# Optimization experiments

Measured on AMD Instinct MI355X. Metric: run time of the kernel, lower is better.

Reference implementation:

```python
import jax, jax.numpy as jnp
import numpy as np

B, T = 4, 8
H, W = 120, 160
NON_SEM = 4
CAT = 16
MAP_CH = NON_SEM + CAT          # 20 map channels
FEAT_CH = 2 * NON_SEM + CAT     # 24 feature channels
RES = 5.0                       # cm per map cell
GLOBAL_M, LOCAL_M = 960, 240    # map_size/resolution, and /downscale
M2 = LOCAL_M * LOCAL_M
HFOV = 79.0
CAM_H_CM = 88.0
VISION_CM = 100 * RES           # vision_range cells -> cm
AGENT_R2 = 2.0 ** 2
EXPLORE_R2 = 3.0 ** 2
FX = W / (2.0 * float(np.tan(np.deg2rad(HFOV) / 2.0)))
FY = FX
CX, CY = W / 2.0, H / 2.0

LOCAL_POSE0 = jnp.array([LOCAL_M * RES / 2, LOCAL_M * RES / 2, 0.0], jnp.float32)
GLOBAL_POSE0 = jnp.array([GLOBAL_M * RES / 2, GLOBAL_M * RES / 2, 0.0], jnp.float32)
OFF = (GLOBAL_M - LOCAL_M) // 2
BOUNDS0 = jnp.array([OFF, OFF + LOCAL_M, OFF, OFF + LOCAL_M], jnp.int32)
ORIGINS0 = jnp.array([OFF * RES, OFF * RES, 0.0], jnp.float32)


def _splat1(flat, w):  # scatter-add scalar weights into the flattened local grid
    return jnp.zeros((M2,), jnp.float32).at[flat].add(w)


def _splatC(flat, vals):  # vals [C, N] -> [C, M2]
    return jnp.zeros((vals.shape[0], M2), jnp.float32).at[:, flat].add(vals)


def _step(carry, xs):
    lmap, gmap, lpose, gpose, bounds, origins = carry
    obs, delta, cam_T, done, upd = xs
    doneb = done != 0
    # per-env reset on episode end (init_map_and_pose_for_env)
    lmap = jnp.where(doneb[:, None, None, None], 0.0, lmap)
    gmap = jnp.where(doneb[:, None, None, None], 0.0, gmap)
    lpose = jnp.where(doneb[:, None], LOCAL_POSE0, lpose)
    gpose = jnp.where(doneb[:, None], GLOBAL_POSE0, gpose)
    bounds = jnp.where(doneb[:, None], BOUNDS0, bounds)
    origins = jnp.where(doneb[:, None], ORIGINS0, origins)

    # dead-reckoning pose update (delta in agent frame)
    th = jnp.deg2rad(lpose[:, 2])
    dx = delta[:, 0] * jnp.cos(th) - delta[:, 1] * jnp.sin(th)
    dy = delta[:, 0] * jnp.sin(th) + delta[:, 1] * jnp.cos(th)
    lpose = lpose + jnp.stack([dx, dy, delta[:, 2]], -1)

    # depth -> camera-frame point cloud (cm)
    depth = obs[:, 3] * 400.0 + 50.0  # [B,H,W]
    sem = obs[:, NON_SEM:]            # [B,CAT,H,W]
    uu = (jnp.arange(W, dtype=jnp.float32) - CX)[None, None, :]
    vv = (CY - jnp.arange(H, dtype=jnp.float32))[None, :, None]
    pts = jnp.stack([uu * depth / FX, vv * depth / FY, depth, jnp.ones_like(depth)], -1)
    pts = jnp.einsum('bij,bhwj->bhwi', cam_T, pts)  # camera extrinsics
    x_f, y_l, z_u = pts[..., 2], -pts[..., 0], pts[..., 1] + CAM_H_CM

    # agent frame -> local map frame
    th2 = jnp.deg2rad(lpose[:, 2])[:, None, None]
    wx = lpose[:, 0][:, None, None] + x_f * jnp.cos(th2) - y_l * jnp.sin(th2)
    wy = lpose[:, 1][:, None, None] + x_f * jnp.sin(th2) + y_l * jnp.cos(th2)
    ix = jnp.floor(wx / RES).astype(jnp.int32)
    iy = jnp.floor(wy / RES).astype(jnp.int32)
    valid = (depth > 25.0) & (depth < VISION_CM) & (ix >= 0) & (ix < LOCAL_M) & (iy >= 0) & (iy < LOCAL_M)
    flat = (jnp.clip(iy, 0, LOCAL_M - 1) * LOCAL_M + jnp.clip(ix, 0, LOCAL_M - 1)).reshape(B, -1)
    vm = valid.reshape(B, -1).astype(jnp.float32)
    obst_w = vm * ((z_u > 25.0) & (z_u < 150.0)).reshape(B, -1).astype(jnp.float32)

    exp_grid = jax.vmap(_splat1)(flat, vm).reshape(B, LOCAL_M, LOCAL_M)
    obst_grid = jax.vmap(_splat1)(flat, obst_w).reshape(B, LOCAL_M, LOCAL_M)
    sem_grid = jax.vmap(_splatC)(flat, sem.reshape(B, CAT, -1) * vm[:, None, :]).reshape(B, CAT, LOCAL_M, LOCAL_M)

    # agent location / been-close disks
    g = jnp.arange(LOCAL_M, dtype=jnp.float32)
    dxg = g[None, None, :] - (lpose[:, 0] / RES)[:, None, None]
    dyg = g[None, :, None] - (lpose[:, 1] / RES)[:, None, None]
    d2 = dxg * dxg + dyg * dyg
    agent = (d2 <= AGENT_R2).astype(jnp.float32)
    close = (d2 <= EXPLORE_R2).astype(jnp.float32)

    lmap = jnp.concatenate([
        jnp.maximum(lmap[:, 0], jnp.clip(obst_grid, 0.0, 1.0))[:, None],
        jnp.maximum(lmap[:, 1], jnp.clip(exp_grid, 0.0, 1.0))[:, None],
        agent[:, None],
        jnp.maximum(lmap[:, 3], close)[:, None],
        jnp.maximum(lmap[:, NON_SEM:], jnp.clip(sem_grid, 0.0, 1.0)),
    ], axis=1)

    # fuse local window into global map for envs flagged for update
    y1, x1 = bounds[:, 0], bounds[:, 2]
    crop = jax.vmap(lambda gm, y, x: jax.lax.dynamic_slice(gm, (0, y, x), (MAP_CH, LOCAL_M, LOCAL_M)))(gmap, y1, x1)
    updb = (upd != 0)[:, None, None, None]
    fused = jnp.where(updb, jnp.maximum(crop, lmap), crop)
    gmap = jax.vmap(lambda gm, c, y, x: jax.lax.dynamic_update_slice(gm, c, (0, y, x)))(gmap, fused, y1, x1)
    gpose = jnp.where((upd != 0)[:, None], lpose + origins, gpose)

    feats = jnp.concatenate([lmap[:, :NON_SEM], fused[:, :NON_SEM], lmap[:, NON_SEM:]], axis=1)
    return (lmap, gmap, lpose, gpose, bounds, origins), (feats, lpose, gpose, bounds, origins)


def _forward(obs_seq, pose_delta, cam_poses, init_local_map, init_global_map,
             init_local_pose, init_global_pose, init_origins,
             done_flags, update_flags, init_bounds):
    xs = (obs_seq.swapaxes(0, 1), pose_delta.swapaxes(0, 1), cam_poses.swapaxes(0, 1),
          done_flags.swapaxes(0, 1), update_flags.swapaxes(0, 1))
    carry0 = (init_local_map, init_global_map, init_local_pose, init_global_pose, init_bounds, init_origins)
    carry, ys = jax.lax.scan(_step, carry0, xs)
    feats, lp, gp, bnds, orgs = ys
    return (feats.swapaxes(0, 1), carry[0], carry[1], lp.swapaxes(0, 1), gp.swapaxes(0, 1),
            bnds.swapaxes(0, 1), orgs.swapaxes(0, 1))


def setup_inputs() -> dict:
    key = jax.random.key(0)
    ks = jax.random.split(key, 5)
    obs_seq = jax.random.uniform(ks[0], (B, T, MAP_CH, H, W), jnp.float32)
    pose_delta = jax.random.normal(ks[1], (B, T, 3), jnp.float32) * jnp.array([10.0, 2.0, 5.0], jnp.float32)
    cam_poses = jnp.eye(4, dtype=jnp.float32)[None, None] + 0.02 * jax.random.normal(ks[2], (B, T, 4, 4), jnp.float32)
    done_flags = jax.random.randint(ks[3], (B, T), 0, 2, jnp.int32)
    update_flags = jax.random.randint(ks[4], (B, T), 0, 2, jnp.int32)
    return {
        'obs_seq': obs_seq,
        'pose_delta': pose_delta,
        'done_flags': done_flags,
        'update_flags': update_flags,
        'cam_poses': cam_poses,
        'init_local_map': jnp.zeros((B, MAP_CH, LOCAL_M, LOCAL_M), jnp.float32),
        'init_global_map': jnp.zeros((B, MAP_CH, GLOBAL_M, GLOBAL_M), jnp.float32),
        'init_local_pose': jnp.tile(LOCAL_POSE0[None], (B, 1)),
        'init_global_pose': jnp.tile(GLOBAL_POSE0[None], (B, 1)),
        'init_bounds': jnp.tile(BOUNDS0[None], (B, 1)),
        'init_origins': jnp.tile(ORIGINS0[None], (B, 1)),
    }


def reference(obs_seq, pose_delta, done_flags, update_flags, cam_poses,
              init_local_map, init_global_map, init_local_pose, init_global_pose,
              init_bounds, init_origins):
    return _forward(obs_seq, pose_delta, cam_poses, init_local_map, init_global_map,
                    init_local_pose, init_global_pose, init_origins,
                    done_flags, update_flags, init_bounds)
```

## Files before the change

kernel.cpp:

```cpp
#include <hip/hip_runtime.h>
#include <math.h>

#define Bn 4
#define Tn 8
#define Hn 120
#define Wn 160
#define HWn (Hn * Wn)
#define NON_SEMn 4
#define CATn 16
#define MAP_CHn 20
#define FEAT_CHn 24
#define LOCAL_Mn 240
#define GLOBAL_Mn 960
#define M2n (LOCAL_Mn * LOCAL_Mn)
#define TBMn (Tn * Bn * M2n)
#define Pn (Tn * Bn * HWn)
#define NBLK_SCAN 1800

#define DEG2RADf ((float)0.017453292519943295)

#define OUT_FEATS 0
#define OUT_LMAP  44236800
#define OUT_GMAP  48844800
#define OUT_LP    122572800
#define OUT_GP    122572896
#define OUT_BNDS  122572992
#define OUT_ORGS  122573120

#define WS_LPOSE  0
#define WS_ANYD   96
#define WS_EXP    128
#define WS_OBST   (WS_EXP + TBMn)
#define WS_CNT    (WS_OBST + TBMn)
#define WS_OFF    (WS_CNT + TBMn)
#define WS_CUR    (WS_OFF + TBMn)
#define WS_BSUM   (WS_CUR + TBMn)
#define WS_CELL   (WS_BSUM + 2048)
#define WS_LIST   (WS_CELL + Pn)
#define WS_REC    (WS_LIST + Pn)


__global__ void pose_kernel(const float* __restrict__ pose_delta,
                            const int* __restrict__ done_flags,
                            const int* __restrict__ upd_flags,
                            const float* __restrict__ init_lpose,
                            const float* __restrict__ init_gpose,
                            const int* __restrict__ init_bounds,
                            const float* __restrict__ init_origins,
                            float* __restrict__ ws_lpose,
                            float* __restrict__ ws_anydone,
                            float* __restrict__ out_lp,
                            float* __restrict__ out_gp,
                            float* __restrict__ out_bnds,
                            float* __restrict__ out_orgs) {
#pragma clang fp contract(off)
    int b = threadIdx.x;
    if (b >= Bn) return;
    float lx = init_lpose[b * 3 + 0], ly = init_lpose[b * 3 + 1], lz = init_lpose[b * 3 + 2];
    float gx = init_gpose[b * 3 + 0], gy = init_gpose[b * 3 + 1], gz = init_gpose[b * 3 + 2];
    int b0 = init_bounds[b * 4 + 0], b1 = init_bounds[b * 4 + 1];
    int b2i = init_bounds[b * 4 + 2], b3 = init_bounds[b * 4 + 3];
    float ox = init_origins[b * 3 + 0], oy = init_origins[b * 3 + 1], oz = init_origins[b * 3 + 2];
    float anyd = 0.0f;
    for (int t = 0; t < Tn; t++) {
        int done = done_flags[b * Tn + t];
        int upd  = upd_flags[b * Tn + t];
        if (done) {
            lx = 600.0f; ly = 600.0f; lz = 0.0f;
            gx = 2400.0f; gy = 2400.0f; gz = 0.0f;
            b0 = 360; b1 = 600; b2i = 360; b3 = 600;
            ox = 1800.0f; oy = 1800.0f; oz = 0.0f;
            anyd = 1.0f;
        }
        float th = lz * DEG2RADf;
        float c = cosf(th), s = sinf(th);
        float d0 = pose_delta[(b * Tn + t) * 3 + 0];
        float d1 = pose_delta[(b * Tn + t) * 3 + 1];
        float d2 = pose_delta[(b * Tn + t) * 3 + 2];
        lx = lx + (d0 * c - d1 * s);
        ly = ly + (d0 * s + d1 * c);
        lz = lz + d2;
        if (upd) { gx = lx + ox; gy = ly + oy; gz = lz + oz; }
        ws_lpose[(t * Bn + b) * 3 + 0] = lx;
        ws_lpose[(t * Bn + b) * 3 + 1] = ly;
        ws_lpose[(t * Bn + b) * 3 + 2] = lz;
        out_lp[(b * Tn + t) * 3 + 0] = lx;
        out_lp[(b * Tn + t) * 3 + 1] = ly;
        out_lp[(b * Tn + t) * 3 + 2] = lz;
        out_gp[(b * Tn + t) * 3 + 0] = gx;
        out_gp[(b * Tn + t) * 3 + 1] = gy;
        out_gp[(b * Tn + t) * 3 + 2] = gz;
        out_bnds[(b * Tn + t) * 4 + 0] = (float)b0;
        out_bnds[(b * Tn + t) * 4 + 1] = (float)b1;
        out_bnds[(b * Tn + t) * 4 + 2] = (float)b2i;
        out_bnds[(b * Tn + t) * 4 + 3] = (float)b3;
        out_orgs[(b * Tn + t) * 3 + 0] = ox;
        out_orgs[(b * Tn + t) * 3 + 1] = oy;
        out_orgs[(b * Tn + t) * 3 + 2] = oz;
    }
    ws_anydone[b] = anyd;
}

__global__ void project_bin_kernel(const float* __restrict__ obs,
                                   const float* __restrict__ cam,
                                   const float* __restrict__ ws_lpose,
                                   float* __restrict__ g_exp,
                                   float* __restrict__ g_obst,
                                   unsigned* __restrict__ cnt,
                                   int* __restrict__ cellid,
                                   float* __restrict__ rec,
                                   float fx) {
#pragma clang fp contract(off)
    int g = blockIdx.x * blockDim.x + threadIdx.x;
    if (g >= Pn) return;
    int p = g % HWn;
    int tb = g / HWn;
    int b = tb % Bn;
    int t = tb / Bn;
    int h = p / Wn, w = p % Wn;
    const float* ob = obs + (size_t)((b * Tn + t) * MAP_CHn) * HWn;
    float depth = ob[3 * HWn + p] * 400.0f + 50.0f;
    float u = (float)w - 80.0f;
    float v = 60.0f - (float)h;
    float px = u * depth / fx;
    float py = v * depth / fx;
    float pz = depth;
    const float* Tm = cam + (size_t)(b * Tn + t) * 16;
    float X = ((Tm[0] * px + Tm[1] * py) + Tm[2] * pz) + Tm[3];
    float Y = ((Tm[4] * px + Tm[5] * py) + Tm[6] * pz) + Tm[7];
    float Z = ((Tm[8] * px + Tm[9] * py) + Tm[10] * pz) + Tm[11];
    float x_f = Z;
    float y_l = -X;
    float z_u = Y + 88.0f;
    float lx = ws_lpose[(t * Bn + b) * 3 + 0];
    float ly = ws_lpose[(t * Bn + b) * 3 + 1];
    float lz = ws_lpose[(t * Bn + b) * 3 + 2];
    float th2 = lz * DEG2RADf;
    float c2 = cosf(th2), s2 = sinf(th2);
    float wx = (lx + x_f * c2) - y_l * s2;
    float wy = (ly + x_f * s2) + y_l * c2;
    int ix = (int)floorf(wx / 5.0f);
    int iy = (int)floorf(wy / 5.0f);
    bool valid = (depth > 25.0f) && (depth < 500.0f) &&
                 (ix >= 0) && (ix < LOCAL_Mn) && (iy >= 0) && (iy < LOCAL_Mn);

    float4 r[4];
#pragma unroll
    for (int q = 0; q < 4; q++) {
        r[q].x = ob[(size_t)(NON_SEMn + 4 * q + 0) * HWn + p];
        r[q].y = ob[(size_t)(NON_SEMn + 4 * q + 1) * HWn + p];
        r[q].z = ob[(size_t)(NON_SEMn + 4 * q + 2) * HWn + p];
        r[q].w = ob[(size_t)(NON_SEMn + 4 * q + 3) * HWn + p];
    }
    float4* rp = (float4*)(rec + (size_t)g * CATn);
#pragma unroll
    for (int q = 0; q < 4; q++) rp[q] = r[q];

    int cell = -1;
    if (valid) {
        cell = (t * Bn + b) * M2n + iy * LOCAL_Mn + ix;
        g_exp[cell] = 1.0f;
        if (z_u > 25.0f && z_u < 150.0f) g_obst[cell] = 1.0f;
        atomicAdd(&cnt[cell], 1u);
    }
    cellid[g] = cell;
}

__global__ void scan1_kernel(const unsigned* __restrict__ cnt,
                             unsigned* __restrict__ off,
                             unsigned* __restrict__ bsum) {
    __shared__ unsigned s[256];
    int tid = threadIdx.x;
    int base = blockIdx.x * 1024 + tid * 4;
    unsigned v0 = cnt[base], v1 = cnt[base + 1], v2 = cnt[base + 2], v3 = cnt[base + 3];
    unsigned tsum = v0 + v1 + v2 + v3;
    s[tid] = tsum;
    __syncthreads();
    for (int d = 1; d < 256; d <<= 1) {
        unsigned a = (tid >= d) ? s[tid - d] : 0u;
        __syncthreads();
        s[tid] += a;
        __syncthreads();
    }
    unsigned excl = s[tid] - tsum;
    if (tid == 255) bsum[blockIdx.x] = s[255];
    off[base]     = excl;
    off[base + 1] = excl + v0;
    off[base + 2] = excl + v0 + v1;
    off[base + 3] = excl + v0 + v1 + v2;
}

__global__ void scan2_kernel(unsigned* __restrict__ bsum) {
    __shared__ unsigned s[256];
    int tid = threadIdx.x;
    unsigned run = 0;
    for (int base = 0; base < NBLK_SCAN; base += 256) {
        int i = base + tid;
        unsigned v = (i < NBLK_SCAN) ? bsum[i] : 0u;
        s[tid] = v;
        __syncthreads();
        for (int d = 1; d < 256; d <<= 1) {
            unsigned a = (tid >= d) ? s[tid - d] : 0u;
            __syncthreads();
            s[tid] += a;
            __syncthreads();
        }
        unsigned tot = s[255];
        if (i < NBLK_SCAN) bsum[i] = run + s[tid] - v;
        run += tot;
        __syncthreads();
    }
}

__global__ void scan3_kernel(unsigned* __restrict__ off,
                             const unsigned* __restrict__ bsum,
                             unsigned* __restrict__ cur) {
    int i = blockIdx.x * blockDim.x + threadIdx.x;
    if (i >= TBMn) return;
    unsigned o = off[i] + bsum[i >> 10];
    off[i] = o;
    cur[i] = o;
}

__global__ void scatter_kernel(const int* __restrict__ cellid,
                               unsigned* __restrict__ cur,
                               unsigned* __restrict__ list) {
    int g = blockIdx.x * blockDim.x + threadIdx.x;
    if (g >= Pn) return;
    int c = cellid[g];
    if (c < 0) return;
    unsigned pos = atomicAdd(&cur[c], 1u);
    list[pos] = (unsigned)g;
}

__global__ void update_kernel(const float* __restrict__ g_exp,
                              const float* __restrict__ g_obst,
                              const unsigned* __restrict__ cnt,
                              const unsigned* __restrict__ off,
                              const unsigned* __restrict__ list,
                              const float* __restrict__ rec,
                              const int* __restrict__ done_flags,
                              const int* __restrict__ upd_flags,
                              const float* __restrict__ ws_lpose,
                              const float* __restrict__ init_lmap,
                              const float* __restrict__ init_gmap,
                              const int* __restrict__ init_bounds,
                              float* __restrict__ out_feats,
                              float* __restrict__ out_lmap,
                              float* __restrict__ out_gmap) {
#pragma clang fp contract(off)
    int idx = blockIdx.x * blockDim.x + threadIdx.x;
    if (idx >= Bn * M2n) return;
    int b = idx / M2n, j = idx % M2n;
    int y = j / LOCAL_Mn, x = j % LOCAL_Mn;
    int y1 = init_bounds[b * 4 + 0];
    int x1 = init_bounds[b * 4 + 2];

    float lm[MAP_CHn], cr[MAP_CHn];
#pragma unroll
    for (int ch = 0; ch < MAP_CHn; ch++)
        lm[ch] = init_lmap[((size_t)(b * MAP_CHn + ch)) * M2n + j];
#pragma unroll
    for (int ch = 0; ch < MAP_CHn; ch++)
        cr[ch] = init_gmap[((size_t)(b * MAP_CHn + ch) * GLOBAL_Mn + (y1 + y)) * GLOBAL_Mn + (x1 + x)];

    for (int t = 0; t < Tn; t++) {
        int done = done_flags[b * Tn + t];
        int upd  = upd_flags[b * Tn + t];
        if (done) {
#pragma unroll
            for (int ch = 0; ch < MAP_CHn; ch++) { lm[ch] = 0.0f; cr[ch] = 0.0f; }
        }
        float lx = ws_lpose[(t * Bn + b) * 3 + 0];
        float ly = ws_lpose[(t * Bn + b) * 3 + 1];
        float dxg = (float)x - lx / 5.0f;
        float dyg = (float)y - ly / 5.0f;
        float d2 = dxg * dxg + dyg * dyg;
        float agent = (d2 <= 4.0f) ? 1.0f : 0.0f;
        float close = (d2 <= 9.0f) ? 1.0f : 0.0f;

        int cell = (t * Bn + b) * M2n + j;
        float expv  = g_exp[cell];
        float obstv = g_obst[cell];
        lm[0] = fmaxf(lm[0], fminf(fmaxf(obstv, 0.0f), 1.0f));
        lm[1] = fmaxf(lm[1], fminf(fmaxf(expv, 0.0f), 1.0f));
        lm[2] = agent;
        lm[3] = fmaxf(lm[3], close);

        float sem[CATn];
#pragma unroll
        for (int c = 0; c < CATn; c++) sem[c] = 0.0f;
        unsigned n = cnt[cell];
        unsigned st = off[cell];
        for (unsigned k = 0; k < n; k++) {
            unsigned g = list[st + k];
            const float4* rp = (const float4*)(rec + (size_t)g * CATn);
            float4 r0 = rp[0], r1 = rp[1], r2 = rp[2], r3 = rp[3];
            sem[0] += r0.x;  sem[1] += r0.y;  sem[2] += r0.z;  sem[3] += r0.w;
            sem[4] += r1.x;  sem[5] += r1.y;  sem[6] += r1.z;  sem[7] += r1.w;
            sem[8] += r2.x;  sem[9] += r2.y;  sem[10] += r2.z; sem[11] += r2.w;
            sem[12] += r3.x; sem[13] += r3.y; sem[14] += r3.z; sem[15] += r3.w;
        }
#pragma unroll
        for (int c = 0; c < CATn; c++)
            lm[NON_SEMn + c] = fmaxf(lm[NON_SEMn + c], fminf(fmaxf(sem[c], 0.0f), 1.0f));
        if (upd) {
#pragma unroll
            for (int ch = 0; ch < MAP_CHn; ch++) cr[ch] = fmaxf(cr[ch], lm[ch]);
        }

        size_t fb = ((size_t)(b * Tn + t) * FEAT_CHn) * M2n + j;
#pragma unroll
        for (int ch = 0; ch < NON_SEMn; ch++) out_feats[fb + (size_t)ch * M2n] = lm[ch];
#pragma unroll
        for (int ch = 0; ch < NON_SEMn; ch++) out_feats[fb + (size_t)(NON_SEMn + ch) * M2n] = cr[ch];
#pragma unroll
        for (int c = 0; c < CATn; c++) out_feats[fb + (size_t)(2 * NON_SEMn + c) * M2n] = lm[NON_SEMn + c];
    }

#pragma unroll
    for (int ch = 0; ch < MAP_CHn; ch++)
        out_lmap[((size_t)(b * MAP_CHn + ch)) * M2n + j] = lm[ch];
#pragma unroll
    for (int ch = 0; ch < MAP_CHn; ch++)
        out_gmap[((size_t)(b * MAP_CHn + ch) * GLOBAL_Mn + (y1 + y)) * GLOBAL_Mn + (x1 + x)] = cr[ch];
}

__global__ void final_gmap_kernel(const float* __restrict__ init_gmap,
                                  const int* __restrict__ init_bounds,
                                  const float* __restrict__ anydone,
                                  float* __restrict__ out_gmap) {
    size_t i4 = (size_t)blockIdx.x * blockDim.x + threadIdx.x;
    const size_t total4 = (size_t)Bn * MAP_CHn * GLOBAL_Mn * GLOBAL_Mn / 4;
    if (i4 >= total4) return;
    size_t f = i4 * 4;
    int gx = (int)(f % GLOBAL_Mn);
    size_t r = f / GLOBAL_Mn;
    int gy = (int)(r % GLOBAL_Mn);
    size_t bc = r / GLOBAL_Mn;
    int b = (int)(bc / MAP_CHn);
    int y1 = init_bounds[b * 4 + 0];
    int x1 = init_bounds[b * 4 + 2];
    if (gy >= y1 && gy < y1 + LOCAL_Mn && gx >= x1 && gx < x1 + LOCAL_Mn) return;
    float4 v;
    if (anydone[b] != 0.0f) {
        v = make_float4(0.0f, 0.0f, 0.0f, 0.0f);
    } else {
        v = *(const float4*)(init_gmap + f);
    }
    *(float4*)(out_gmap + f) = v;
}

extern "C" void kernel_launch(void* const* d_in, const int* in_sizes, int n_in,
                              void* d_out, int out_size, void* d_ws, size_t ws_size,
                              hipStream_t stream) {
    const float* obs        = (const float*)d_in[0];
    const float* pose_delta = (const float*)d_in[1];
    const int*   done_flags = (const int*)d_in[2];
    const int*   upd_flags  = (const int*)d_in[3];
    const float* cam_poses  = (const float*)d_in[4];
    const float* init_lmap  = (const float*)d_in[5];
    const float* init_gmap  = (const float*)d_in[6];
    const float* init_lpose = (const float*)d_in[7];
    const float* init_gpose = (const float*)d_in[8];
    const int*   init_bnds  = (const int*)d_in[9];
    const float* init_orgs  = (const float*)d_in[10];

    float* out = (float*)d_out;
    float* ws  = (float*)d_ws;

    float*    ws_lpose = ws + WS_LPOSE;
    float*    ws_anyd  = ws + WS_ANYD;
    float*    g_exp    = ws + WS_EXP;
    float*    g_obst   = ws + WS_OBST;
    unsigned* cnt      = (unsigned*)(ws + WS_CNT);
    unsigned* off      = (unsigned*)(ws + WS_OFF);
    unsigned* cur      = (unsigned*)(ws + WS_CUR);
    unsigned* bsum     = (unsigned*)(ws + WS_BSUM);
    int*      cellid   = (int*)(ws + WS_CELL);
    unsigned* list     = (unsigned*)(ws + WS_LIST);
    float*    rec      = ws + WS_REC;

    float fx = (float)(160.0 / (2.0 * tan(79.0 * M_PI / 180.0 / 2.0)));

    pose_kernel<<<1, 64, 0, stream>>>(pose_delta, done_flags, upd_flags,
                                      init_lpose, init_gpose, init_bnds, init_orgs,
                                      ws_lpose, ws_anyd,
                                      out + OUT_LP, out + OUT_GP,
                                      out + OUT_BNDS, out + OUT_ORGS);

    hipMemsetAsync(g_exp, 0, (size_t)3 * TBMn * sizeof(float), stream);

    project_bin_kernel<<<(Pn + 255) / 256, 256, 0, stream>>>(
        obs, cam_poses, ws_lpose, g_exp, g_obst, cnt, cellid, rec, fx);

    scan1_kernel<<<NBLK_SCAN, 256, 0, stream>>>(cnt, off, bsum);
    scan2_kernel<<<1, 256, 0, stream>>>(bsum);
    scan3_kernel<<<(TBMn + 255) / 256, 256, 0, stream>>>(off, bsum, cur);

    scatter_kernel<<<(Pn + 255) / 256, 256, 0, stream>>>(cellid, cur, list);

    update_kernel<<<(Bn * M2n + 255) / 256, 256, 0, stream>>>(
        g_exp, g_obst, cnt, off, list, rec, done_flags, upd_flags, ws_lpose,
        init_lmap, init_gmap, init_bnds,
        out + OUT_FEATS, out + OUT_LMAP, out + OUT_GMAP);

    const size_t gmap_total4 = (size_t)Bn * MAP_CHn * GLOBAL_Mn * GLOBAL_Mn / 4;
    final_gmap_kernel<<<(int)((gmap_total4 + 255) / 256), 256, 0, stream>>>(
        init_gmap, init_bnds, ws_anyd, out + OUT_GMAP);
}
```

Baseline: 925.5 us.

## Pack per-cell state into uint4, fuse scan stages and gmap copy into one kernel

Packs the per-cell explored, obstacle, count and offset values into one 16-byte record, so the update kernel reads a single vector load per cell instead of four scattered arrays. The three-stage scan becomes two kernels: each block now sums its predecessors' totals itself. The full global-map copy is merged into the update kernel as extra blocks, cutting launches and letting both run concurrently. Nontemporal loads and stores are added for the large streaming traffic, at the cost of redundant prefix sums per block and possible cache-policy side effects.

```diff
diff --git a/kernel.cpp b/kernel.cpp
--- a/kernel.cpp
+++ b/kernel.cpp
@@ -16,8 +16,12 @@
 #define TBMn (Tn * Bn * M2n)
 #define Pn (Tn * Bn * HWn)
 #define NBLK_SCAN 1800
+#define UPD_BLKS ((Bn * M2n + 255) / 256)
+#define GMAP_BLKS ((Bn * MAP_CHn * GLOBAL_Mn * GLOBAL_Mn / 4 + 255) / 256)
 
 #define DEG2RADf ((float)0.017453292519943295)
+
+typedef float vf4 __attribute__((ext_vector_type(4)));
 
 #define OUT_FEATS 0
 #define OUT_LMAP  44236800
@@ -29,15 +33,11 @@
 
 #define WS_LPOSE  0
 #define WS_ANYD   96
-#define WS_EXP    128
-#define WS_OBST   (WS_EXP + TBMn)
-#define WS_CNT    (WS_OBST + TBMn)
-#define WS_OFF    (WS_CNT + TBMn)
-#define WS_CUR    (WS_OFF + TBMn)
-#define WS_BSUM   (WS_CUR + TBMn)
+#define WS_REC4   128
+#define WS_BSUM   (WS_REC4 + 4 * TBMn)
 #define WS_CELL   (WS_BSUM + 2048)
 #define WS_LIST   (WS_CELL + Pn)
-#define WS_REC    (WS_LIST + Pn)
+#define WS_RECS   (WS_LIST + Pn)
 
 
 __global__ void pose_kernel(const float* __restrict__ pose_delta,
@@ -104,11 +104,9 @@
 __global__ void project_bin_kernel(const float* __restrict__ obs,
                                    const float* __restrict__ cam,
                                    const float* __restrict__ ws_lpose,
-                                   float* __restrict__ g_exp,
-                                   float* __restrict__ g_obst,
-                                   unsigned* __restrict__ cnt,
+                                   uint4* __restrict__ rec4,
                                    int* __restrict__ cellid,
-                                   float* __restrict__ rec,
+                                   float* __restrict__ recs,
                                    float fx) {
 #pragma clang fp contract(off)
     int g = blockIdx.x * blockDim.x + threadIdx.x;
@@ -144,7 +142,7 @@
     bool valid = (depth > 25.0f) && (depth < 500.0f) &&
                  (ix >= 0) && (ix < LOCAL_Mn) && (iy >= 0) && (iy < LOCAL_Mn);
 
-    float4 r[4];
+    vf4 r[4];
 #pragma unroll
     for (int q = 0; q < 4; q++) {
         r[q].x = ob[(size_t)(NON_SEMn + 4 * q + 0) * HWn + p];
@@ -152,27 +150,29 @@
         r[q].z = ob[(size_t)(NON_SEMn + 4 * q + 2) * HWn + p];
         r[q].w = ob[(size_t)(NON_SEMn + 4 * q + 3) * HWn + p];
     }
-    float4* rp = (float4*)(rec + (size_t)g * CATn);
-#pragma unroll
-    for (int q = 0; q < 4; q++) rp[q] = r[q];
+    vf4* rp = (vf4*)(recs + (size_t)g * CATn);
+#pragma unroll
+    for (int q = 0; q < 4; q++)
+        __builtin_nontemporal_store(r[q], rp + q);
 
     int cell = -1;
     if (valid) {
         cell = (t * Bn + b) * M2n + iy * LOCAL_Mn + ix;
-        g_exp[cell] = 1.0f;
-        if (z_u > 25.0f && z_u < 150.0f) g_obst[cell] = 1.0f;
-        atomicAdd(&cnt[cell], 1u);
+        float* rf = (float*)&rec4[cell];
+        rf[0] = 1.0f;
+        if (z_u > 25.0f && z_u < 150.0f) rf[1] = 1.0f;
+        atomicAdd(((unsigned*)&rec4[cell]) + 2, 1u);
     }
     cellid[g] = cell;
 }
 
-__global__ void scan1_kernel(const unsigned* __restrict__ cnt,
-                             unsigned* __restrict__ off,
+__global__ void scan1_kernel(uint4* __restrict__ rec4,
                              unsigned* __restrict__ bsum) {
     __shared__ unsigned s[256];
     int tid = threadIdx.x;
     int base = blockIdx.x * 1024 + tid * 4;
-    unsigned v0 = cnt[base], v1 = cnt[base + 1], v2 = cnt[base + 2], v3 = cnt[base + 3];
+    uint4 r0 = rec4[base], r1 = rec4[base + 1], r2 = rec4[base + 2], r3 = rec4[base + 3];
+    unsigned v0 = r0.z, v1 = r1.z, v2 = r2.z, v3 = r3.z;
     unsigned tsum = v0 + v1 + v2 + v3;
     s[tid] = tsum;
     __syncthreads();
@@ -184,71 +184,83 @@
     }
     unsigned excl = s[tid] - tsum;
     if (tid == 255) bsum[blockIdx.x] = s[255];
-    off[base]     = excl;
-    off[base + 1] = excl + v0;
-    off[base + 2] = excl + v0 + v1;
-    off[base + 3] = excl + v0 + v1 + v2;
-}
-
-__global__ void scan2_kernel(unsigned* __restrict__ bsum) {
-    __shared__ unsigned s[256];
+    ((unsigned*)&rec4[base])[3]     = excl;
+    ((unsigned*)&rec4[base + 1])[3] = excl + v0;
+    ((unsigned*)&rec4[base + 2])[3] = excl + v0 + v1;
+    ((unsigned*)&rec4[base + 3])[3] = excl + v0 + v1 + v2;
+}
+
+__global__ void scan_carry_kernel(uint4* __restrict__ rec4,
+                                  const unsigned* __restrict__ bsum) {
+    __shared__ unsigned ls[256];
     int tid = threadIdx.x;
-    unsigned run = 0;
-    for (int base = 0; base < NBLK_SCAN; base += 256) {
-        int i = base + tid;
-        unsigned v = (i < NBLK_SCAN) ? bsum[i] : 0u;
-        s[tid] = v;
+    unsigned part = 0;
+    for (int i = tid; i < (int)blockIdx.x; i += 256) part += bsum[i];
+    ls[tid] = part;
+    __syncthreads();
+    for (int d = 128; d > 0; d >>= 1) {
+        if (tid < d) ls[tid] += ls[tid + d];
         __syncthreads();
-        for (int d = 1; d < 256; d <<= 1) {
-            unsigned a = (tid >= d) ? s[tid - d] : 0u;
-            __syncthreads();
-            s[tid] += a;
-            __syncthreads();
-        }
-        unsigned tot = s[255];
-        if (i < NBLK_SCAN) bsum[i] = run + s[tid] - v;
-        run += tot;
-        __syncthreads();
-    }
-}
-
-__global__ void scan3_kernel(unsigned* __restrict__ off,
-                             const unsigned* __restrict__ bsum,
-                             unsigned* __restrict__ cur) {
-    int i = blockIdx.x * blockDim.x + threadIdx.x;
-    if (i >= TBMn) return;
-    unsigned o = off[i] + bsum[i >> 10];
-    off[i] = o;
-    cur[i] = o;
+    }
+    unsigned carry = ls[0];
+    if (carry == 0) return;
+    int base = blockIdx.x * 1024 + tid * 4;
+#pragma unroll
+    for (int k = 0; k < 4; k++) {
+        unsigned* wp = ((unsigned*)&rec4[base + k]) + 3;
+        *wp = *wp + carry;
+    }
 }
 
 __global__ void scatter_kernel(const int* __restrict__ cellid,
-                               unsigned* __restrict__ cur,
+                               uint4* __restrict__ rec4,
                                unsigned* __restrict__ list) {
     int g = blockIdx.x * blockDim.x + threadIdx.x;
     if (g >= Pn) return;
     int c = cellid[g];
     if (c < 0) return;
-    unsigned pos = atomicAdd(&cur[c], 1u);
+    unsigned pos = atomicAdd(((unsigned*)&rec4[c]) + 3, 1u);
     list[pos] = (unsigned)g;
 }
 
-__global__ void update_kernel(const float* __restrict__ g_exp,
-                              const float* __restrict__ g_obst,
-                              const unsigned* __restrict__ cnt,
-                              const unsigned* __restrict__ off,
-                              const unsigned* __restrict__ list,
-                              const float* __restrict__ rec,
-                              const int* __restrict__ done_flags,
-                              const int* __restrict__ upd_flags,
-                              const float* __restrict__ ws_lpose,
-                              const float* __restrict__ init_lmap,
-                              const float* __restrict__ init_gmap,
-                              const int* __restrict__ init_bounds,
-                              float* __restrict__ out_feats,
-                              float* __restrict__ out_lmap,
-                              float* __restrict__ out_gmap) {
+__global__ void __launch_bounds__(256)
+mega_kernel(const uint4* __restrict__ rec4,
+            const unsigned* __restrict__ list,
+            const float* __restrict__ recs,
+            const int* __restrict__ done_flags,
+            const int* __restrict__ upd_flags,
+            const float* __restrict__ ws_lpose,
+            const float* __restrict__ init_lmap,
+            const float* __restrict__ init_gmap,
+            const int* __restrict__ init_bounds,
+            const float* __restrict__ anydone,
+            float* __restrict__ out_feats,
+            float* __restrict__ out_lmap,
+            float* __restrict__ out_gmap) {
 #pragma clang fp contract(off)
+    if (blockIdx.x >= UPD_BLKS) {
+        size_t i4 = (size_t)(blockIdx.x - UPD_BLKS) * blockDim.x + threadIdx.x;
+        const size_t total4 = (size_t)Bn * MAP_CHn * GLOBAL_Mn * GLOBAL_Mn / 4;
+        if (i4 >= total4) return;
+        size_t f = i4 * 4;
+        int gx = (int)(f % GLOBAL_Mn);
+        size_t r = f / GLOBAL_Mn;
+        int gy = (int)(r % GLOBAL_Mn);
+        size_t bc = r / GLOBAL_Mn;
+        int b = (int)(bc / MAP_CHn);
+        int y1 = init_bounds[b * 4 + 0];
+        int x1 = init_bounds[b * 4 + 2];
+        if (gy >= y1 && gy < y1 + LOCAL_Mn && gx >= x1 && gx < x1 + LOCAL_Mn) return;
+        vf4 v;
+        if (anydone[b] != 0.0f) {
+            v = (vf4)(0.0f);
+        } else {
+            v = __builtin_nontemporal_load((const vf4*)(init_gmap + f));
+        }
+        __builtin_nontemporal_store(v, (vf4*)(out_gmap + f));
+        return;
+    }
+
     int idx = blockIdx.x * blockDim.x + threadIdx.x;
     if (idx >= Bn * M2n) return;
     int b = idx / M2n, j = idx % M2n;
@@ -259,10 +271,11 @@
     float lm[MAP_CHn], cr[MAP_CHn];
 #pragma unroll
     for (int ch = 0; ch < MAP_CHn; ch++)
-        lm[ch] = init_lmap[((size_t)(b * MAP_CHn + ch)) * M2n + j];
+        lm[ch] = __builtin_nontemporal_load(init_lmap + ((size_t)(b * MAP_CHn + ch)) * M2n + j);
 #pragma unroll
     for (int ch = 0; ch < MAP_CHn; ch++)
-        cr[ch] = init_gmap[((size_t)(b * MAP_CHn + ch) * GLOBAL_Mn + (y1 + y)) * GLOBAL_Mn + (x1 + x)];
+        cr[ch] = __builtin_nontemporal_load(
+            init_gmap + ((size_t)(b * MAP_CHn + ch) * GLOBAL_Mn + (y1 + y)) * GLOBAL_Mn + (x1 + x));
 
     for (int t = 0; t < Tn; t++) {
         int done = done_flags[b * Tn + t];
@@ -280,8 +293,11 @@
         float close = (d2 <= 9.0f) ? 1.0f : 0.0f;
 
         int cell = (t * Bn + b) * M2n + j;
-        float expv  = g_exp[cell];
-        float obstv = g_obst[cell];
+        uint4 rc = rec4[cell];
+        float expv  = __uint_as_float(rc.x);
+        float obstv = __uint_as_float(rc.y);
+        unsigned n  = rc.z;
+        unsigned st = rc.w - n;
         lm[0] = fmaxf(lm[0], fminf(fmaxf(obstv, 0.0f), 1.0f));
         lm[1] = fmaxf(lm[1], fminf(fmaxf(expv, 0.0f), 1.0f));
         lm[2] = agent;
@@ -290,12 +306,10 @@
         float sem[CATn];
 #pragma unroll
         for (int c = 0; c < CATn; c++) sem[c] = 0.0f;
-        unsigned n = cnt[cell];
-        unsigned st = off[cell];
         for (unsigned k = 0; k < n; k++) {
             unsigned g = list[st + k];
-            const float4* rp = (const float4*)(rec + (size_t)g * CATn);
-            float4 r0 = rp[0], r1 = rp[1], r2 = rp[2], r3 = rp[3];
+            const vf4* rp = (const vf4*)(recs + (size_t)g * CATn);
+            vf4 r0 = rp[0], r1 = rp[1], r2 = rp[2], r3 = rp[3];
             sem[0] += r0.x;  sem[1] += r0.y;  sem[2] += r0.z;  sem[3] += r0.w;
             sem[4] += r1.x;  sem[5] += r1.y;  sem[6] += r1.z;  sem[7] += r1.w;
             sem[8] += r2.x;  sem[9] += r2.y;  sem[10] += r2.z; sem[11] += r2.w;
@@ -311,44 +325,23 @@
 
         size_t fb = ((size_t)(b * Tn + t) * FEAT_CHn) * M2n + j;
 #pragma unroll
-        for (int ch = 0; ch < NON_SEMn; ch++) out_feats[fb + (size_t)ch * M2n] = lm[ch];
-#pragma unroll
-        for (int ch = 0; ch < NON_SEMn; ch++) out_feats[fb + (size_t)(NON_SEMn + ch) * M2n] = cr[ch];
-#pragma unroll
-        for (int c = 0; c < CATn; c++) out_feats[fb + (size_t)(2 * NON_SEMn + c) * M2n] = lm[NON_SEMn + c];
+        for (int ch = 0; ch < NON_SEMn; ch++)
+            __builtin_nontemporal_store(lm[ch], out_feats + fb + (size_t)ch * M2n);
+#pragma unroll
+        for (int ch = 0; ch < NON_SEMn; ch++)
+            __builtin_nontemporal_store(cr[ch], out_feats + fb + (size_t)(NON_SEMn + ch) * M2n);
+#pragma unroll
+        for (int c = 0; c < CATn; c++)
+            __builtin_nontemporal_store(lm[NON_SEMn + c], out_feats + fb + (size_t)(2 * NON_SEMn + c) * M2n);
     }
 
 #pragma unroll
     for (int ch = 0; ch < MAP_CHn; ch++)
-        out_lmap[((size_t)(b * MAP_CHn + ch)) * M2n + j] = lm[ch];
+        __builtin_nontemporal_store(lm[ch], out_lmap + ((size_t)(b * MAP_CHn + ch)) * M2n + j);
 #pragma unroll
     for (int ch = 0; ch < MAP_CHn; ch++)
-        out_gmap[((size_t)(b * MAP_CHn + ch) * GLOBAL_Mn + (y1 + y)) * GLOBAL_Mn + (x1 + x)] = cr[ch];
-}
-
-__global__ void final_gmap_kernel(const float* __restrict__ init_gmap,
-                                  const int* __restrict__ init_bounds,
-                                  const float* __restrict__ anydone,
-                                  float* __restrict__ out_gmap) {
-    size_t i4 = (size_t)blockIdx.x * blockDim.x + threadIdx.x;
-    const size_t total4 = (size_t)Bn * MAP_CHn * GLOBAL_Mn * GLOBAL_Mn / 4;
-    if (i4 >= total4) return;
-    size_t f = i4 * 4;
-    int gx = (int)(f % GLOBAL_Mn);
-    size_t r = f / GLOBAL_Mn;
-    int gy = (int)(r % GLOBAL_Mn);
-    size_t bc = r / GLOBAL_Mn;
-    int b = (int)(bc / MAP_CHn);
-    int y1 = init_bounds[b * 4 + 0];
-    int x1 = init_bounds[b * 4 + 2];
-    if (gy >= y1 && gy < y1 + LOCAL_Mn && gx >= x1 && gx < x1 + LOCAL_Mn) return;
-    float4 v;
-    if (anydone[b] != 0.0f) {
-        v = make_float4(0.0f, 0.0f, 0.0f, 0.0f);
-    } else {
-        v = *(const float4*)(init_gmap + f);
-    }
-    *(float4*)(out_gmap + f) = v;
+        __builtin_nontemporal_store(
+            cr[ch], out_gmap + ((size_t)(b * MAP_CHn + ch) * GLOBAL_Mn + (y1 + y)) * GLOBAL_Mn + (x1 + x));
 }
 
 extern "C" void kernel_launch(void* const* d_in, const int* in_sizes, int n_in,
@@ -371,15 +364,11 @@
 
     float*    ws_lpose = ws + WS_LPOSE;
     float*    ws_anyd  = ws + WS_ANYD;
-    float*    g_exp    = ws + WS_EXP;
-    float*    g_obst   = ws + WS_OBST;
-    unsigned* cnt      = (unsigned*)(ws + WS_CNT);
-    unsigned* off      = (unsigned*)(ws + WS_OFF);
-    unsigned* cur      = (unsigned*)(ws + WS_CUR);
+    uint4*    rec4     = (uint4*)(ws + WS_REC4);
     unsigned* bsum     = (unsigned*)(ws + WS_BSUM);
     int*      cellid   = (int*)(ws + WS_CELL);
     unsigned* list     = (unsigned*)(ws + WS_LIST);
-    float*    rec      = ws + WS_REC;
+    float*    recs     = ws + WS_RECS;
 
     float fx = (float)(160.0 / (2.0 * tan(79.0 * M_PI / 180.0 / 2.0)));
 
@@ -389,23 +378,18 @@
                                       out + OUT_LP, out + OUT_GP,
                                       out + OUT_BNDS, out + OUT_ORGS);
 
-    hipMemsetAsync(g_exp, 0, (size_t)3 * TBMn * sizeof(float), stream);
+    (void)hipMemsetAsync(rec4, 0, (size_t)TBMn * sizeof(uint4), stream);
 
     project_bin_kernel<<<(Pn + 255) / 256, 256, 0, stream>>>(
-        obs, cam_poses, ws_lpose, g_exp, g_obst, cnt, cellid, rec, fx);
-
-    scan1_kernel<<<NBLK_SCAN, 256, 0, stream>>>(cnt, off, bsum);
-    scan2_kernel<<<1, 256, 0, stream>>>(bsum);
-    scan3_kernel<<<(TBMn + 255) / 256, 256, 0, stream>>>(off, bsum, cur);
-
-    scatter_kernel<<<(Pn + 255) / 256, 256, 0, stream>>>(cellid, cur, list);
-
-    update_kernel<<<(Bn * M2n + 255) / 256, 256, 0, stream>>>(
-        g_exp, g_obst, cnt, off, list, rec, done_flags, upd_flags, ws_lpose,
-        init_lmap, init_gmap, init_bnds,
+        obs, cam_poses, ws_lpose, rec4, cellid, recs, fx);
+
+    scan1_kernel<<<NBLK_SCAN, 256, 0, stream>>>(rec4, bsum);
+    scan_carry_kernel<<<NBLK_SCAN, 256, 0, stream>>>(rec4, bsum);
+
+    scatter_kernel<<<(Pn + 255) / 256, 256, 0, stream>>>(cellid, rec4, list);
+
+    mega_kernel<<<UPD_BLKS + GMAP_BLKS, 256, 0, stream>>>(
+        rec4, list, recs, done_flags, upd_flags, ws_lpose,
+        init_lmap, init_gmap, init_bnds, ws_anyd,
         out + OUT_FEATS, out + OUT_LMAP, out + OUT_GMAP);
-
-    const size_t gmap_total4 = (size_t)Bn * MAP_CHn * GLOBAL_Mn * GLOBAL_Mn / 4;
-    final_gmap_kernel<<<(int)((gmap_total4 + 255) / 256), 256, 0, stream>>>(
-        init_gmap, init_bnds, ws_anyd, out + OUT_GMAP);
-}
+}
```

After: 920.9 us. About the same (-0.5%).
